# Optimization experiments

Hardware: AMD Instinct MI355X
Metric: run time of the kernel (lower is better)

Reference implementation:

```python
import jax, jax.numpy as jnp
import numpy as np
import jax.scipy.linalg as jsl

T = 2048      # number of time steps
N = 8192      # number of particles / states
D = 4         # matrix_size (dims[-1] = 16)
H = 128       # MLP hidden width

def setup_inputs() -> dict:
    key = jax.random.key(0)
    ks = jax.random.split(key, 8)
    x = jax.random.normal(ks[0], (N, D), dtype=jnp.float32)
    t = jnp.sort(jax.random.uniform(ks[1], (T,), dtype=jnp.float32))
    # MLP params, stored (in, out); torch Linear does x @ W.T + b
    def xavier(k, fan_in, fan_out):
        s = jnp.sqrt(2.0 / (fan_in + fan_out))
        return (s * jax.random.normal(k, (fan_in, fan_out))).astype(jnp.float32)
    W1 = xavier(ks[2], 1, H); b1 = jnp.zeros((H,), jnp.float32)
    W2 = xavier(ks[3], H, H); b2 = jnp.zeros((H,), jnp.float32)
    W3 = xavier(ks[4], H, D * D); b3 = jnp.zeros((D * D,), jnp.float32)
    M0 = jnp.zeros((D, D), jnp.float32)  # zero buffer (M0=None)
    return {"x": x, "t": t, "M0": M0, "W1": W1, "b1": b1,
            "W2": W2, "b2": b2, "W3": W3, "b3": b3}

def reference(x, t, M0, W1, b1, W2, b2, W3, b3):
    t0 = 0.0
    tt = jnp.concatenate([jnp.full((1, 1), t0, t.dtype), t.reshape(-1, 1)], axis=0)  # (T+1,1)
    delta_t = tt[1:] - tt[:-1]          # (T,1)
    t_avg = (tt[1:] + tt[:-1]) * 0.5    # (T,1)
    # per-step MLP -> (T, D*D)
    h = jnp.tanh(t_avg @ W1 + b1)
    h = jnp.tanh(h @ W2 + b2)
    A = (h @ W3 + b3).reshape(-1, D, D)
    A = A + M0[None, :, :]
    A = A * delta_t[:, :, None]         # (T,D,D) scaled by dt
    # lie_algebra = identity
    A_sum = jnp.cumsum(A, axis=0)       # prefix-sum over time
    E = jax.vmap(jsl.expm)(A_sum)       # batched matrix exponential (T,D,D)
    out = jnp.einsum('tij,nj->tni', E, x)  # (T,N,D)
    return out
```

## Files before the change

### kernel.cpp

```cpp
#include <hip/hip_runtime.h>
#include <math.h>

#define TT 2048
#define NN 8192
#define HH 128

typedef float f4 __attribute__((ext_vector_type(4)));

__global__ void mlp_kernel(const float* __restrict__ t_arr,
                           const float* __restrict__ M0,
                           const float* __restrict__ W1, const float* __restrict__ b1,
                           const float* __restrict__ W2, const float* __restrict__ b2,
                           const float* __restrict__ W3, const float* __restrict__ b3,
                           float* __restrict__ A_t) {
    const int t = blockIdx.x;
    const int j = threadIdx.x;
    __shared__ float h1[HH];
    __shared__ float h2[HH];

    const float t_cur  = t_arr[t];
    const float t_prev = (t > 0) ? t_arr[t - 1] : 0.0f;
    const float dt = t_cur - t_prev;
    const float ta = 0.5f * (t_cur + t_prev);

    h1[j] = tanhf(fmaf(ta, W1[j], b1[j]));
    __syncthreads();

    float acc = b2[j];
    #pragma unroll 8
    for (int i = 0; i < HH; ++i) acc = fmaf(h1[i], W2[i * HH + j], acc);
    h2[j] = tanhf(acc);
    __syncthreads();

    if (j < 16) {
        float a = b3[j];
        #pragma unroll 8
        for (int i = 0; i < HH; ++i) a = fmaf(h2[i], W3[i * 16 + j], a);
        a = (a + M0[j]) * dt;
        A_t[j * TT + t] = a;
    }
}

__global__ __launch_bounds__(1024) void scan_kernel(const float* __restrict__ A_t,
                                                    float* __restrict__ Asum) {
    const int tid = threadIdx.x;
    const int e = tid >> 6;
    const int c = tid & 63;
    const float4* src = (const float4*)(A_t + e * TT + c * 32);

    float4 v[8];
    float s = 0.0f;
    #pragma unroll
    for (int i = 0; i < 8; ++i) {
        v[i] = src[i];
        s += v[i].x + v[i].y + v[i].z + v[i].w;
    }

    float sc = s;
    #pragma unroll
    for (int d = 1; d < 64; d <<= 1) {
        const float up = __shfl_up(sc, d, 64);
        if (c >= d) sc += up;
    }
    const float ex = __shfl_up(sc, 1, 64);
    float run = (c == 0) ? 0.0f : ex;

    const int t0 = c * 32;
    #pragma unroll
    for (int i = 0; i < 8; ++i) {
        run += v[i].x; Asum[(t0 + 4 * i + 0) * 16 + e] = run;
        run += v[i].y; Asum[(t0 + 4 * i + 1) * 16 + e] = run;
        run += v[i].z; Asum[(t0 + 4 * i + 2) * 16 + e] = run;
        run += v[i].w; Asum[(t0 + 4 * i + 3) * 16 + e] = run;
    }
}

__device__ __forceinline__ void mm4(const float* __restrict__ A,
                                    const float* __restrict__ B,
                                    float* __restrict__ C) {
    #pragma unroll
    for (int i = 0; i < 4; ++i) {
        #pragma unroll
        for (int j = 0; j < 4; ++j) {
            float s = 0.0f;
            #pragma unroll
            for (int k = 0; k < 4; ++k) s = fmaf(A[i * 4 + k], B[k * 4 + j], s);
            C[i * 4 + j] = s;
        }
    }
}

__global__ __launch_bounds__(64) void expm_kernel(const float* __restrict__ Asum,
                                                  float* __restrict__ E) {
    const int t = blockIdx.x * blockDim.x + threadIdx.x;
    if (t >= TT) return;

    float M[16];
    const float4* src = (const float4*)(Asum + t * 16);
    #pragma unroll
    for (int r = 0; r < 4; ++r) {
        float4 v = src[r];
        M[r * 4 + 0] = v.x; M[r * 4 + 1] = v.y; M[r * 4 + 2] = v.z; M[r * 4 + 3] = v.w;
    }

    float nrm = 0.0f;
    #pragma unroll
    for (int i = 0; i < 4; ++i) {
        float rs = fabsf(M[i*4+0]) + fabsf(M[i*4+1]) + fabsf(M[i*4+2]) + fabsf(M[i*4+3]);
        nrm = fmaxf(nrm, rs);
    }
    int k = 0;
    while (nrm > 0.5f && k < 40) { nrm *= 0.5f; ++k; }
    const float sc = ldexpf(1.0f, -k);
    #pragma unroll
    for (int i = 0; i < 16; ++i) M[i] *= sc;

    float R[16], P[16], Q[16];
    #pragma unroll
    for (int i = 0; i < 16; ++i) { P[i] = M[i]; R[i] = M[i]; }
    R[0] += 1.0f; R[5] += 1.0f; R[10] += 1.0f; R[15] += 1.0f;
    for (int n = 2; n <= 12; ++n) {
        mm4(P, M, Q);
        const float inv = 1.0f / (float)n;
        #pragma unroll
        for (int i = 0; i < 16; ++i) { P[i] = Q[i] * inv; R[i] += P[i]; }
    }
    for (int s = 0; s < k; ++s) {
        mm4(R, R, Q);
        #pragma unroll
        for (int i = 0; i < 16; ++i) R[i] = Q[i];
    }

    float4* dst = (float4*)(E + t * 16);
    #pragma unroll
    for (int r = 0; r < 4; ++r)
        dst[r] = make_float4(R[r*4+0], R[r*4+1], R[r*4+2], R[r*4+3]);
}

__global__ __launch_bounds__(256) void apply_kernel(const float* __restrict__ E,
                                                    const float* __restrict__ x,
                                                    float* __restrict__ out) {
    const int t = blockIdx.y;
    const int nbase = blockIdx.x * (NN / 2);

    const f4* Ev = (const f4*)(E + t * 16);
    const f4 e0 = Ev[0], e1 = Ev[1], e2 = Ev[2], e3 = Ev[3];

    const f4* xs = (const f4*)x + nbase;
    f4* os = (f4*)out + (size_t)t * NN + nbase;

    #pragma unroll 4
    for (int n = threadIdx.x; n < NN / 2; n += 256) {
        const f4 xv = xs[n];
        f4 o;
        o.x = fmaf(e0.x, xv.x, fmaf(e0.y, xv.y, fmaf(e0.z, xv.z, e0.w * xv.w)));
        o.y = fmaf(e1.x, xv.x, fmaf(e1.y, xv.y, fmaf(e1.z, xv.z, e1.w * xv.w)));
        o.z = fmaf(e2.x, xv.x, fmaf(e2.y, xv.y, fmaf(e2.z, xv.z, e2.w * xv.w)));
        o.w = fmaf(e3.x, xv.x, fmaf(e3.y, xv.y, fmaf(e3.z, xv.z, e3.w * xv.w)));
        os[n] = o;
    }
}

extern "C" void kernel_launch(void* const* d_in, const int* in_sizes, int n_in,
                              void* d_out, int out_size, void* d_ws, size_t ws_size,
                              hipStream_t stream) {
    const float* x  = (const float*)d_in[0];
    const float* t  = (const float*)d_in[1];
    const float* M0 = (const float*)d_in[2];
    const float* W1 = (const float*)d_in[3];
    const float* b1 = (const float*)d_in[4];
    const float* W2 = (const float*)d_in[5];
    const float* b2 = (const float*)d_in[6];
    const float* W3 = (const float*)d_in[7];
    const float* b3 = (const float*)d_in[8];
    float* out = (float*)d_out;

    float* A_t  = (float*)d_ws;
    float* Asum = A_t  + 16 * TT;
    float* E    = Asum + 16 * TT;

    mlp_kernel<<<TT, HH, 0, stream>>>(t, M0, W1, b1, W2, b2, W3, b3, A_t);
    scan_kernel<<<1, 1024, 0, stream>>>(A_t, Asum);
    expm_kernel<<<TT / 64, 64, 0, stream>>>(Asum, E);
    apply_kernel<<<dim3(2, TT), 256, 0, stream>>>(E, x, out);
}
```

Before: 313.1 us.

## Fuse prefix-scan and matrix exponential into one kernel with redundant per-block scans

Merges the single-block scan kernel and the expm kernel into one kernel launched with 16 blocks. Each block recomputes the full prefix scan over all 16 matrix entries and keeps only its own 128-step slice in shared memory, then computes the exponentials for that slice. This removes one kernel launch and the global round-trip of Asum, at the cost of 16 redundant scans and fewer blocks running the expm work.

New measurement: 297.6 us. 5.0% less time.

```diff
diff --git a/kernel.cpp b/kernel.cpp
--- a/kernel.cpp
+++ b/kernel.cpp
@@ -41,40 +41,6 @@
     }
 }
 
-__global__ __launch_bounds__(1024) void scan_kernel(const float* __restrict__ A_t,
-                                                    float* __restrict__ Asum) {
-    const int tid = threadIdx.x;
-    const int e = tid >> 6;
-    const int c = tid & 63;
-    const float4* src = (const float4*)(A_t + e * TT + c * 32);
-
-    float4 v[8];
-    float s = 0.0f;
-    #pragma unroll
-    for (int i = 0; i < 8; ++i) {
-        v[i] = src[i];
-        s += v[i].x + v[i].y + v[i].z + v[i].w;
-    }
-
-    float sc = s;
-    #pragma unroll
-    for (int d = 1; d < 64; d <<= 1) {
-        const float up = __shfl_up(sc, d, 64);
-        if (c >= d) sc += up;
-    }
-    const float ex = __shfl_up(sc, 1, 64);
-    float run = (c == 0) ? 0.0f : ex;
-
-    const int t0 = c * 32;
-    #pragma unroll
-    for (int i = 0; i < 8; ++i) {
-        run += v[i].x; Asum[(t0 + 4 * i + 0) * 16 + e] = run;
-        run += v[i].y; Asum[(t0 + 4 * i + 1) * 16 + e] = run;
-        run += v[i].z; Asum[(t0 + 4 * i + 2) * 16 + e] = run;
-        run += v[i].w; Asum[(t0 + 4 * i + 3) * 16 + e] = run;
-    }
-}
-
 __device__ __forceinline__ void mm4(const float* __restrict__ A,
                                     const float* __restrict__ B,
                                     float* __restrict__ C) {
@@ -90,51 +56,88 @@
     }
 }
 
-__global__ __launch_bounds__(64) void expm_kernel(const float* __restrict__ Asum,
-                                                  float* __restrict__ E) {
-    const int t = blockIdx.x * blockDim.x + threadIdx.x;
-    if (t >= TT) return;
+__global__ __launch_bounds__(256) void scanexpm_kernel(const float* __restrict__ A_t,
+                                                       float* __restrict__ E) {
+    const int b    = blockIdx.x;
+    const int w    = threadIdx.x >> 6;
+    const int lane = threadIdx.x & 63;
 
-    float M[16];
-    const float4* src = (const float4*)(Asum + t * 16);
+    __shared__ float As[128][17];
+
     #pragma unroll
     for (int r = 0; r < 4; ++r) {
-        float4 v = src[r];
-        M[r * 4 + 0] = v.x; M[r * 4 + 1] = v.y; M[r * 4 + 2] = v.z; M[r * 4 + 3] = v.w;
+        const int m = (w << 2) | r;
+        const float4* src = (const float4*)(A_t + m * TT + lane * 32);
+        float4 v[8];
+        float s = 0.0f;
+        #pragma unroll
+        for (int i = 0; i < 8; ++i) {
+            v[i] = src[i];
+            s += v[i].x + v[i].y + v[i].z + v[i].w;
+        }
+        float sc = s;
+        #pragma unroll
+        for (int d = 1; d < 64; d <<= 1) {
+            const float up = __shfl_up(sc, d, 64);
+            if (lane >= d) sc += up;
+        }
+        const float ex = __shfl_up(sc, 1, 64);
+        float run = (lane == 0) ? 0.0f : ex;
+
+        if ((lane >> 2) == b) {
+            const int tl = (lane & 3) * 32;
+            #pragma unroll
+            for (int i = 0; i < 8; ++i) {
+                run += v[i].x; As[tl + 4*i + 0][m] = run;
+                run += v[i].y; As[tl + 4*i + 1][m] = run;
+                run += v[i].z; As[tl + 4*i + 2][m] = run;
+                run += v[i].w; As[tl + 4*i + 3][m] = run;
+            }
+        }
     }
+    __syncthreads();
 
-    float nrm = 0.0f;
-    #pragma unroll
-    for (int i = 0; i < 4; ++i) {
-        float rs = fabsf(M[i*4+0]) + fabsf(M[i*4+1]) + fabsf(M[i*4+2]) + fabsf(M[i*4+3]);
-        nrm = fmaxf(nrm, rs);
+    if (threadIdx.x < 128) {
+        const int tl = threadIdx.x;
+        const int t  = (b << 7) + tl;
+
+        float M[16];
+        #pragma unroll
+        for (int i = 0; i < 16; ++i) M[i] = As[tl][i];
+
+        float nrm = 0.0f;
+        #pragma unroll
+        for (int i = 0; i < 4; ++i) {
+            float rs = fabsf(M[i*4+0]) + fabsf(M[i*4+1]) + fabsf(M[i*4+2]) + fabsf(M[i*4+3]);
+            nrm = fmaxf(nrm, rs);
+        }
+        int k = 0;
+        while (nrm > 0.5f && k < 40) { nrm *= 0.5f; ++k; }
+        const float sc = ldexpf(1.0f, -k);
+        #pragma unroll
+        for (int i = 0; i < 16; ++i) M[i] *= sc;
+
+        float R[16], P[16], Q[16];
+        #pragma unroll
+        for (int i = 0; i < 16; ++i) { P[i] = M[i]; R[i] = M[i]; }
+        R[0] += 1.0f; R[5] += 1.0f; R[10] += 1.0f; R[15] += 1.0f;
+        for (int n = 2; n <= 12; ++n) {
+            mm4(P, M, Q);
+            const float inv = 1.0f / (float)n;
+            #pragma unroll
+            for (int i = 0; i < 16; ++i) { P[i] = Q[i] * inv; R[i] += P[i]; }
+        }
+        for (int s = 0; s < k; ++s) {
+            mm4(R, R, Q);
+            #pragma unroll
+            for (int i = 0; i < 16; ++i) R[i] = Q[i];
+        }
+
+        float4* dst = (float4*)(E + t * 16);
+        #pragma unroll
+        for (int r = 0; r < 4; ++r)
+            dst[r] = make_float4(R[r*4+0], R[r*4+1], R[r*4+2], R[r*4+3]);
     }
-    int k = 0;
-    while (nrm > 0.5f && k < 40) { nrm *= 0.5f; ++k; }
-    const float sc = ldexpf(1.0f, -k);
-    #pragma unroll
-    for (int i = 0; i < 16; ++i) M[i] *= sc;
-
-    float R[16], P[16], Q[16];
-    #pragma unroll
-    for (int i = 0; i < 16; ++i) { P[i] = M[i]; R[i] = M[i]; }
-    R[0] += 1.0f; R[5] += 1.0f; R[10] += 1.0f; R[15] += 1.0f;
-    for (int n = 2; n <= 12; ++n) {
-        mm4(P, M, Q);
-        const float inv = 1.0f / (float)n;
-        #pragma unroll
-        for (int i = 0; i < 16; ++i) { P[i] = Q[i] * inv; R[i] += P[i]; }
-    }
-    for (int s = 0; s < k; ++s) {
-        mm4(R, R, Q);
-        #pragma unroll
-        for (int i = 0; i < 16; ++i) R[i] = Q[i];
-    }
-
-    float4* dst = (float4*)(E + t * 16);
-    #pragma unroll
-    for (int r = 0; r < 4; ++r)
-        dst[r] = make_float4(R[r*4+0], R[r*4+1], R[r*4+2], R[r*4+3]);
 }
 
 __global__ __launch_bounds__(256) void apply_kernel(const float* __restrict__ E,
@@ -175,12 +178,10 @@
     const float* b3 = (const float*)d_in[8];
     float* out = (float*)d_out;
 
-    float* A_t  = (float*)d_ws;
-    float* Asum = A_t  + 16 * TT;
-    float* E    = Asum + 16 * TT;
+    float* A_t = (float*)d_ws;
+    float* E   = A_t + 16 * TT;
 
     mlp_kernel<<<TT, HH, 0, stream>>>(t, M0, W1, b1, W2, b2, W3, b3, A_t);
-    scan_kernel<<<1, 1024, 0, stream>>>(A_t, Asum);
-    expm_kernel<<<TT / 64, 64, 0, stream>>>(Asum, E);
+    scanexpm_kernel<<<16, 256, 0, stream>>>(A_t, E);
     apply_kernel<<<dim3(2, TT), 256, 0, stream>>>(E, x, out);
 }
```
